# Performance work log

Hardware: AMD Instinct MI355X
Metric: run time of the kernel (lower is better)

## Reference

```python
import jax, jax.numpy as jnp
import numpy as np

D = 128
HIDDEN = 512
N = 2048


def setup_inputs() -> dict:
    key = jax.random.key(0)
    k_x, k0, k1, k2 = jax.random.split(key, 4)
    x = jax.random.normal(k_x, (N, D), dtype=jnp.float32)
    # LocallyConnected init: uniform(-sqrt(1/in), sqrt(1/in))
    b0 = 1.0 / np.sqrt(D)
    b1 = 1.0 / np.sqrt(HIDDEN)
    W0 = jax.random.uniform(k0, (D, D, HIDDEN), jnp.float32, -b0, b0)
    W1 = jax.random.uniform(k1, (D, HIDDEN, HIDDEN), jnp.float32, -b1, b1)
    W2 = jax.random.uniform(k2, (D, HIDDEN, 1), jnp.float32, -b1, b1)
    return {"x": x, "W0": W0, "W1": W1, "W2": W2}


def reference(x, W0, W1, W2):
    n, d = x.shape
    # masking layer: matmul with diag(mask[i]) == elementwise zero-out of diagonal
    mask = 1.0 - jnp.eye(d, dtype=x.dtype)          # [d, d]
    h = x[:, None, :] * mask[None, :, :]            # [n, d, d]
    # per-node locally-connected MLP
    h = jax.nn.leaky_relu(jnp.einsum('ndi,dio->ndo', h, W0))   # [n, d, hidden]
    h = jax.nn.leaky_relu(jnp.einsum('ndi,dio->ndo', h, W1))   # [n, d, hidden]
    h = jnp.einsum('ndi,dio->ndo', h, W2)                      # [n, d, 1]
    return h.squeeze(-1)                                       # [n, d]
```

## Files before the change

### kernel.cpp

```cpp
#include <hip/hip_runtime.h>

#define DD 128
#define HH 512
#define NN 2048
#define NT 64
#define H1_LD 520
#define PLD 516

typedef __bf16 bf16x8 __attribute__((ext_vector_type(8)));
typedef __bf16 bf16x4 __attribute__((ext_vector_type(4)));
typedef float  floatx4 __attribute__((ext_vector_type(4)));

__global__ void cvt_x(const float* __restrict__ x, __bf16* __restrict__ xb) {
    int t = blockIdx.x * blockDim.x + threadIdx.x;
    float4 v = *(const float4*)(x + (size_t)t * 4);
    bf16x4 o;
    o[0] = (__bf16)v.x; o[1] = (__bf16)v.y; o[2] = (__bf16)v.z; o[3] = (__bf16)v.w;
    *(bf16x4*)(xb + (size_t)t * 4) = o;
}

__global__ void pack_w(const float* __restrict__ W, __bf16* __restrict__ Wp, int nks) {
    __shared__ __bf16 Ls[32 * PLD];
    const int d  = blockIdx.x / nks;
    const int ks = blockIdx.x % nks;
    const int tid = threadIdx.x;
    const float* src = W + ((size_t)(d * nks + ks) * 32) * HH;

#pragma unroll
    for (int it = 0; it < 16; ++it) {
        int e = (it * 256 + tid) * 4;
        float4 v = *(const float4*)(src + e);
        bf16x4 o;
        o[0] = (__bf16)v.x; o[1] = (__bf16)v.y; o[2] = (__bf16)v.z; o[3] = (__bf16)v.w;
        *(bf16x4*)(Ls + (e >> 9) * PLD + (e & 511)) = o;
    }
    __syncthreads();

#pragma unroll
    for (int it = 0; it < 8; ++it) {
        int ch = it * 256 + tid;
        int c  = ch & 15;
        int q  = (ch >> 4) & 3;
        int ct = ch >> 6;
        bf16x8 v;
#pragma unroll
        for (int j = 0; j < 8; ++j)
            v[j] = Ls[(q * 8 + j) * PLD + ct * 16 + c];
        *(bf16x8*)(Wp + ((size_t)(d * 32 + ct) * nks + ks) * 512 + (ch & 63) * 8) = v;
    }
}

__launch_bounds__(512, 4)
__global__ void grandag_main(const __bf16* __restrict__ xb,
                             const __bf16* __restrict__ W0p,
                             const __bf16* __restrict__ W1p,
                             const float* __restrict__ W2,
                             float* __restrict__ out) {
    __shared__ __bf16 h1s[NT * H1_LD];
    __shared__ float  outp[NT];

    const int b  = blockIdx.x;
    const int d  = ((b >> 8) << 3) | (b & 7);
    const int t  = (b >> 3) & 31;
    const int n0 = t * NT;

    const int tid = threadIdx.x;
    const int w   = tid >> 6;
    const int l   = tid & 63;
    const int lc  = l & 15;
    const int lq  = l >> 4;

    const int ksz = d >> 5;
    const int lqz = (d >> 3) & 3;
    const int jz  = d & 7;

    if (tid < NT) outp[tid] = 0.f;

    {
        floatx4 acc[4][4] = {};
#pragma unroll
        for (int ks = 0; ks < 4; ks++) {
            bf16x8 af[4], bfm[4];
#pragma unroll
            for (int rt = 0; rt < 4; rt++)
                af[rt] = *(const bf16x8*)(xb + (size_t)(n0 + 16 * rt + lc) * DD + ks * 32 + lq * 8);
            if (ks == ksz && lq == lqz) {
#pragma unroll
                for (int rt = 0; rt < 4; rt++)
#pragma unroll
                    for (int j = 0; j < 8; j++)
                        if (j == jz) af[rt][j] = (__bf16)0.f;
            }
#pragma unroll
            for (int ct = 0; ct < 4; ct++)
                bfm[ct] = *(const bf16x8*)(W0p +
                    ((((size_t)d * 32 + (w * 4 + ct)) * 4 + ks) * 64 + lq * 16 + lc) * 8);
#pragma unroll
            for (int rt = 0; rt < 4; rt++)
#pragma unroll
                for (int ct = 0; ct < 4; ct++)
                    acc[rt][ct] = __builtin_amdgcn_mfma_f32_16x16x32_bf16(
                        af[rt], bfm[ct], acc[rt][ct], 0, 0, 0);
        }
#pragma unroll
        for (int rt = 0; rt < 4; rt++)
#pragma unroll
            for (int ct = 0; ct < 4; ct++)
#pragma unroll
                for (int g = 0; g < 4; g++) {
                    float v = acc[rt][ct][g];
                    v = v > 0.f ? v : 0.01f * v;
                    h1s[(16 * rt + lq * 4 + g) * H1_LD + w * 64 + 16 * ct + lc] = (__bf16)v;
                }
    }
    __syncthreads();

    floatx4 acc2[4][4] = {};
#pragma unroll
    for (int ks = 0; ks < 16; ks++) {
        bf16x8 af[4], bfm[4];
#pragma unroll
        for (int rt = 0; rt < 4; rt++)
            af[rt] = *(const bf16x8*)(h1s + (16 * rt + lc) * H1_LD + ks * 32 + lq * 8);
#pragma unroll
        for (int ct = 0; ct < 4; ct++)
            bfm[ct] = *(const bf16x8*)(W1p +
                ((((size_t)d * 32 + (w * 4 + ct)) * 16 + ks) * 64 + lq * 16 + lc) * 8);
#pragma unroll
        for (int rt = 0; rt < 4; rt++)
#pragma unroll
            for (int ct = 0; ct < 4; ct++)
                acc2[rt][ct] = __builtin_amdgcn_mfma_f32_16x16x32_bf16(
                    af[rt], bfm[ct], acc2[rt][ct], 0, 0, 0);
    }

    float w2v[4];
#pragma unroll
    for (int ct = 0; ct < 4; ct++)
        w2v[ct] = W2[(size_t)d * HH + w * 64 + 16 * ct + lc];
#pragma unroll
    for (int rt = 0; rt < 4; rt++)
#pragma unroll
        for (int g = 0; g < 4; g++) {
            float s = 0.f;
#pragma unroll
            for (int ct = 0; ct < 4; ct++) {
                float v = acc2[rt][ct][g];
                v = v > 0.f ? v : 0.01f * v;
                s += v * w2v[ct];
            }
            s += __shfl_xor(s, 1, 64);
            s += __shfl_xor(s, 2, 64);
            s += __shfl_xor(s, 4, 64);
            s += __shfl_xor(s, 8, 64);
            if (lc == 0) atomicAdd(&outp[16 * rt + lq * 4 + g], s);
        }
    __syncthreads();
    if (tid < NT) out[(size_t)(n0 + tid) * DD + d] = outp[tid];
}

extern "C" void kernel_launch(void* const* d_in, const int* in_sizes, int n_in,
                              void* d_out, int out_size, void* d_ws, size_t ws_size,
                              hipStream_t stream) {
    const float* x  = (const float*)d_in[0];
    const float* W0 = (const float*)d_in[1];
    const float* W1 = (const float*)d_in[2];
    const float* W2 = (const float*)d_in[3];
    float* out = (float*)d_out;

    __bf16* W0p = (__bf16*)d_ws;
    __bf16* W1p = (__bf16*)((char*)d_ws + (size_t)DD * DD * HH * 2);
    __bf16* xb  = (__bf16*)((char*)d_ws + (size_t)DD * DD * HH * 2
                                        + (size_t)DD * HH * HH * 2);

    cvt_x<<<dim3(NN * DD / (256 * 4)), 256, 0, stream>>>(x, xb);
    pack_w<<<dim3(DD * (DD / 32)), 256, 0, stream>>>(W0, W0p, DD / 32);
    pack_w<<<dim3(DD * (HH / 32)), 256, 0, stream>>>(W1, W1p, HH / 32);

    grandag_main<<<dim3(DD * (NN / NT)), 512, 0, stream>>>(xb, W0p, W1p, W2, out);
}
```

Baseline: 432.4 us.

## Transpose MFMA operands, swizzle h1 shared layout, shrink final reduction

The MFMA operands are swapped so weights become the A operand and activations the B operand, which makes each lane's accumulator hold four consecutive hidden outputs. The h1 tile is then written as packed bf16x4 stores into an XOR-swizzled shared layout without padding, replacing scalar bf16 stores, and is read back with the matching swizzle. The W2 epilogue now reduces over the four accumulator elements per lane and needs only two cross-lane shuffles per tile instead of four shuffles per element. The aim is to cut LDS store instructions, bank conflicts and shuffle/atomic overhead, at the cost of more complex indexing.

```diff
diff --git a/kernel.cpp b/kernel.cpp
--- a/kernel.cpp
+++ b/kernel.cpp
@@ -4,7 +4,6 @@
 #define HH 512
 #define NN 2048
 #define NT 64
-#define H1_LD 520
 #define PLD 516
 
 typedef __bf16 bf16x8 __attribute__((ext_vector_type(8)));
@@ -56,19 +55,19 @@
                              const __bf16* __restrict__ W1p,
                              const float* __restrict__ W2,
                              float* __restrict__ out) {
-    __shared__ __bf16 h1s[NT * H1_LD];
+    __shared__ __bf16 h1s[NT * HH];
     __shared__ float  outp[NT];
 
     const int b  = blockIdx.x;
     const int d  = ((b >> 8) << 3) | (b & 7);
-    const int t  = (b >> 3) & 31;
-    const int n0 = t * NT;
+    const int n0 = ((b >> 3) & 31) * NT;
 
     const int tid = threadIdx.x;
     const int w   = tid >> 6;
     const int l   = tid & 63;
     const int lc  = l & 15;
     const int lq  = l >> 4;
+    const int sw  = lc & 7;
 
     const int ksz = d >> 5;
     const int lqz = (d >> 3) & 3;
@@ -80,81 +79,82 @@
         floatx4 acc[4][4] = {};
 #pragma unroll
         for (int ks = 0; ks < 4; ks++) {
-            bf16x8 af[4], bfm[4];
+            bf16x8 xf[4], wf[4];
 #pragma unroll
-            for (int rt = 0; rt < 4; rt++)
-                af[rt] = *(const bf16x8*)(xb + (size_t)(n0 + 16 * rt + lc) * DD + ks * 32 + lq * 8);
+            for (int nt = 0; nt < 4; nt++)
+                xf[nt] = *(const bf16x8*)(xb + (size_t)(n0 + 16 * nt + lc) * DD + ks * 32 + lq * 8);
             if (ks == ksz && lq == lqz) {
 #pragma unroll
-                for (int rt = 0; rt < 4; rt++)
+                for (int nt = 0; nt < 4; nt++)
 #pragma unroll
                     for (int j = 0; j < 8; j++)
-                        if (j == jz) af[rt][j] = (__bf16)0.f;
+                        if (j == jz) xf[nt][j] = (__bf16)0.f;
             }
 #pragma unroll
-            for (int ct = 0; ct < 4; ct++)
-                bfm[ct] = *(const bf16x8*)(W0p +
-                    ((((size_t)d * 32 + (w * 4 + ct)) * 4 + ks) * 64 + lq * 16 + lc) * 8);
+            for (int mt = 0; mt < 4; mt++)
+                wf[mt] = *(const bf16x8*)(W0p +
+                    ((((size_t)d * 32 + (w * 4 + mt)) * 4 + ks) * 64 + lq * 16 + lc) * 8);
 #pragma unroll
-            for (int rt = 0; rt < 4; rt++)
+            for (int mt = 0; mt < 4; mt++)
 #pragma unroll
-                for (int ct = 0; ct < 4; ct++)
-                    acc[rt][ct] = __builtin_amdgcn_mfma_f32_16x16x32_bf16(
-                        af[rt], bfm[ct], acc[rt][ct], 0, 0, 0);
+                for (int nt = 0; nt < 4; nt++)
+                    acc[mt][nt] = __builtin_amdgcn_mfma_f32_16x16x32_bf16(
+                        wf[mt], xf[nt], acc[mt][nt], 0, 0, 0);
         }
 #pragma unroll
-        for (int rt = 0; rt < 4; rt++)
+        for (int mt = 0; mt < 4; mt++) {
+            int chunk = 8 * w + 2 * mt + (lq >> 1);
 #pragma unroll
-            for (int ct = 0; ct < 4; ct++)
+            for (int nt = 0; nt < 4; nt++) {
+                bf16x4 o;
 #pragma unroll
                 for (int g = 0; g < 4; g++) {
-                    float v = acc[rt][ct][g];
-                    v = v > 0.f ? v : 0.01f * v;
-                    h1s[(16 * rt + lq * 4 + g) * H1_LD + w * 64 + 16 * ct + lc] = (__bf16)v;
+                    float v = acc[mt][nt][g];
+                    o[g] = (__bf16)fmaxf(v, 0.01f * v);
                 }
+                *(bf16x4*)(h1s + (16 * nt + lc) * HH + ((chunk ^ sw) << 3) + ((lq & 1) << 2)) = o;
+            }
+        }
     }
     __syncthreads();
 
     floatx4 acc2[4][4] = {};
 #pragma unroll
     for (int ks = 0; ks < 16; ks++) {
-        bf16x8 af[4], bfm[4];
+        bf16x8 hf[4], wf[4];
 #pragma unroll
-        for (int rt = 0; rt < 4; rt++)
-            af[rt] = *(const bf16x8*)(h1s + (16 * rt + lc) * H1_LD + ks * 32 + lq * 8);
+        for (int nt = 0; nt < 4; nt++)
+            hf[nt] = *(const bf16x8*)(h1s + (16 * nt + lc) * HH + (((4 * ks + lq) ^ sw) << 3));
 #pragma unroll
-        for (int ct = 0; ct < 4; ct++)
-            bfm[ct] = *(const bf16x8*)(W1p +
-                ((((size_t)d * 32 + (w * 4 + ct)) * 16 + ks) * 64 + lq * 16 + lc) * 8);
+        for (int mt = 0; mt < 4; mt++)
+            wf[mt] = *(const bf16x8*)(W1p +
+                ((((size_t)d * 32 + (w * 4 + mt)) * 16 + ks) * 64 + lq * 16 + lc) * 8);
 #pragma unroll
-        for (int rt = 0; rt < 4; rt++)
+        for (int mt = 0; mt < 4; mt++)
 #pragma unroll
-            for (int ct = 0; ct < 4; ct++)
-                acc2[rt][ct] = __builtin_amdgcn_mfma_f32_16x16x32_bf16(
-                    af[rt], bfm[ct], acc2[rt][ct], 0, 0, 0);
+            for (int nt = 0; nt < 4; nt++)
+                acc2[mt][nt] = __builtin_amdgcn_mfma_f32_16x16x32_bf16(
+                    wf[mt], hf[nt], acc2[mt][nt], 0, 0, 0);
     }
 
-    float w2v[4];
+    floatx4 w2v[4];
 #pragma unroll
-    for (int ct = 0; ct < 4; ct++)
-        w2v[ct] = W2[(size_t)d * HH + w * 64 + 16 * ct + lc];
+    for (int mt = 0; mt < 4; mt++)
+        w2v[mt] = *(const floatx4*)(W2 + (size_t)d * HH + w * 64 + mt * 16 + lq * 4);
 #pragma unroll
-    for (int rt = 0; rt < 4; rt++)
+    for (int nt = 0; nt < 4; nt++) {
+        float s = 0.f;
 #pragma unroll
-        for (int g = 0; g < 4; g++) {
-            float s = 0.f;
+        for (int mt = 0; mt < 4; mt++)
 #pragma unroll
-            for (int ct = 0; ct < 4; ct++) {
-                float v = acc2[rt][ct][g];
-                v = v > 0.f ? v : 0.01f * v;
-                s += v * w2v[ct];
+            for (int g = 0; g < 4; g++) {
+                float v = acc2[mt][nt][g];
+                s += fmaxf(v, 0.01f * v) * w2v[mt][g];
             }
-            s += __shfl_xor(s, 1, 64);
-            s += __shfl_xor(s, 2, 64);
-            s += __shfl_xor(s, 4, 64);
-            s += __shfl_xor(s, 8, 64);
-            if (lc == 0) atomicAdd(&outp[16 * rt + lq * 4 + g], s);
-        }
+        s += __shfl_xor(s, 16, 64);
+        s += __shfl_xor(s, 32, 64);
+        if (l < 16) atomicAdd(&outp[16 * nt + lc], s);
+    }
     __syncthreads();
     if (tid < NT) out[(size_t)(n0 + tid) * DD + d] = outp[tid];
 }
```

New measurement: 457.5 us. 5.8% more time.
